# Kernel optimization log

Hardware: AMD Instinct MI355X
Metric: run time of the kernel (lower is better)

Reference implementation:

```python
import jax, jax.numpy as jnp
import numpy as np

EPS = 1e-5

def layernorm(x, g, b):
    mu = jnp.mean(x, axis=-1, keepdims=True)
    var = jnp.mean((x - mu) ** 2, axis=-1, keepdims=True)
    return (x - mu) * jax.lax.rsqrt(var + EPS) * g + b

def cswin_attn(q, k, v, lepe_w, lepe_b, H, W, H_sp, W_sp, num_heads):
    # q,k,v: (B, L, C) with C = branch dim
    B, L, C = q.shape
    d = C // num_heads
    nH, nW = H // H_sp, W // W_sp
    def to_win(t):
        t = t.transpose(0, 2, 1).reshape(B, C, nH, H_sp, nW, W_sp)
        t = t.transpose(0, 2, 4, 3, 5, 1).reshape(B * nH * nW, H_sp * W_sp, num_heads, d)
        return t.transpose(0, 2, 1, 3)  # (Bw, h, N, d)
    kw = to_win(k)
    vw = to_win(v)
    # q windows as images for LePE depthwise conv
    qi = q.transpose(0, 2, 1).reshape(B, C, nH, H_sp, nW, W_sp)
    qi = qi.transpose(0, 2, 4, 1, 3, 5).reshape(B * nH * nW, C, H_sp, W_sp)
    lepe = jax.lax.conv_general_dilated(qi, lepe_w, (1, 1), 'SAME',
                                        feature_group_count=C,
                                        dimension_numbers=('NCHW', 'OIHW', 'NCHW'))
    lepe = lepe + lepe_b[None, :, None, None]
    lepe = lepe.reshape(-1, num_heads, d, H_sp * W_sp).transpose(0, 1, 3, 2)
    qw = qi.reshape(-1, num_heads, d, H_sp * W_sp).transpose(0, 1, 3, 2) * (float(d) ** -0.5)
    attn = jax.nn.softmax(jnp.einsum('whnd,whmd->whnm', qw, kw), axis=-1)
    out = jnp.einsum('whnm,whmd->whnd', attn, vw) + lepe  # (Bw, h, N, d)
    out = out.transpose(0, 2, 1, 3).reshape(B, nH, nW, H_sp, W_sp, C)
    out = out.transpose(0, 1, 3, 2, 4, 5).reshape(B, H * W, C)
    return out

def setup_inputs() -> dict:
    key = jax.random.key(0)
    ks = jax.random.split(key, 20)
    B, C, H, W = 8, 128, 64, 64
    ch_z = 512
    hid = 4 * C
    Cb = C // 2  # branch dim
    s = lambda fin: (1.0 / np.sqrt(fin))
    inp = {
        'x': jax.random.normal(ks[0], (B, C, H, W), jnp.float32),
        'z': jax.random.normal(ks[1], (B, ch_z), jnp.float32),
        'ln1_g': jnp.ones((C,), jnp.float32), 'ln1_b': jnp.zeros((C,), jnp.float32),
        'ln2_g': jnp.ones((C,), jnp.float32), 'ln2_b': jnp.zeros((C,), jnp.float32),
        'Wz1': jax.random.normal(ks[2], (C, ch_z), jnp.float32) * s(ch_z),
        'Wz2': jax.random.normal(ks[3], (C, ch_z), jnp.float32) * s(ch_z),
        'Wqkv': jax.random.normal(ks[4], (3 * C, C), jnp.float32) * s(C),
        'Wproj': jax.random.normal(ks[5], (C, C), jnp.float32) * s(C),
        'bproj': jnp.zeros((C,), jnp.float32),
        'lepe_w0': jax.random.normal(ks[6], (Cb, 1, 3, 3), jnp.float32) * (1.0 / 3.0),
        'lepe_b0': jnp.zeros((Cb,), jnp.float32),
        'lepe_w1': jax.random.normal(ks[7], (Cb, 1, 3, 3), jnp.float32) * (1.0 / 3.0),
        'lepe_b1': jnp.zeros((Cb,), jnp.float32),
        'W1': jax.random.normal(ks[8], (hid, C), jnp.float32) * s(C),
        'b1': jnp.zeros((hid,), jnp.float32),
        'W2': jax.random.normal(ks[9], (C, hid), jnp.float32) * s(hid),
        'b2': jnp.zeros((C,), jnp.float32),
    }
    return inp

def reference(x, z, ln1_g, ln1_b, ln2_g, ln2_b, Wz1, Wz2, Wqkv, Wproj, bproj,
              lepe_w0, lepe_b0, lepe_w1, lepe_b1, W1, b1, W2, b2):
    B, C, H, W = x.shape
    nh = 4  # num_heads // 2 per branch
    ss = 8  # split_size
    Cb = C // 2
    xf = x.reshape(B, C, H * W).transpose(0, 2, 1)  # (B, L, C)
    # code-conditioned attention branch
    z1 = z @ Wz1.T  # (B, C)
    h1 = layernorm(xf, ln1_g, ln1_b) + z1[:, None, :]
    qkv = (h1 @ Wqkv.T).reshape(B, H * W, 3, C).transpose(2, 0, 1, 3)  # (3, B, L, C)
    q, k, v = qkv[0], qkv[1], qkv[2]
    x1 = cswin_attn(q[..., :Cb], k[..., :Cb], v[..., :Cb], lepe_w0, lepe_b0, H, W, H, ss, nh)
    x2 = cswin_attn(q[..., Cb:], k[..., Cb:], v[..., Cb:], lepe_w1, lepe_b1, H, W, ss, W, nh)
    att = jnp.concatenate([x1, x2], axis=2) @ Wproj.T + bproj
    xf = xf + att
    # code-conditioned MLP branch
    z2 = z @ Wz2.T
    h2 = layernorm(xf, ln2_g, ln2_b) + z2[:, None, :]
    mlp = jax.nn.gelu(h2 @ W1.T + b1, approximate=False) @ W2.T + b2
    xf = xf + mlp
    return xf.transpose(0, 2, 1).reshape(B, C, H, W)
```

## Files before the change

### kernel.cpp

```cpp
#include <hip/hip_runtime.h>
#include <cstddef>

__device__ __forceinline__ float b2f(unsigned short u) {
  return __uint_as_float(((unsigned int)u) << 16);
}
__device__ __forceinline__ unsigned short f2b(float f) {
  unsigned int u = __float_as_uint(f);
  u = u + 0x7FFFu + ((u >> 16) & 1u);
  return (unsigned short)(u >> 16);
}
__device__ __forceinline__ unsigned int cvtpk(float lo, float hi) {
  unsigned int r;
  asm("v_cvt_pk_bf16_f32 %0, %1, %2" : "=v"(r) : "v"(lo), "v"(hi));
  return r;
}
__device__ __forceinline__ float gelu_exact(float x) {
  return 0.5f * x * (1.0f + erff(x * 0.70710678118654752f));
}

#if defined(__has_builtin)
#if __has_builtin(__builtin_amdgcn_exp2f)
#define EXP2(x) __builtin_amdgcn_exp2f(x)
#else
#define EXP2(x) __expf((x) * 0.6931471805599453f)
#endif
#else
#define EXP2(x) __expf((x) * 0.6931471805599453f)
#endif

typedef __attribute__((ext_vector_type(8))) short bf16x8;
typedef __attribute__((ext_vector_type(4))) short bf16x4;
typedef __attribute__((ext_vector_type(4))) float f32x4;

#if defined(__has_builtin)
#if __has_builtin(__builtin_amdgcn_mfma_f32_16x16x16bf16_1k)
#define MFMA16(a, b, c) __builtin_amdgcn_mfma_f32_16x16x16bf16_1k(a, b, c, 0, 0, 0)
#define HAVE_MFMA16 1
#elif __has_builtin(__builtin_amdgcn_mfma_f32_16x16x16_bf16)
#define MFMA16(a, b, c) __builtin_amdgcn_mfma_f32_16x16x16_bf16(a, b, c, 0, 0, 0)
#define HAVE_MFMA16 1
#endif
#endif

__device__ __forceinline__ unsigned int dtype_flag(const unsigned short* gref) {
  return (gref[0] == 0x3F80u) ? 1u : 0u;
}

struct Ptrs18 { const void* p[18]; };
__constant__ const int c_off[19] = {
    0, 4096, 4224, 4352, 4480, 4608, 70144, 135680, 184832, 201216,
    201344, 201920, 201984, 202560, 202624, 268160, 268672, 334208, 334336};

__global__ __launch_bounds__(256) void k_front(Ptrs18 ptrs,
                                               unsigned short* __restrict__ dst,
                                               const void* __restrict__ x,
                                               const unsigned short* __restrict__ gref,
                                               float* __restrict__ xf) {
  __shared__ float t[32][33];
  int bx = blockIdx.x;
  if (bx < 1306) {
    int idx = bx * 256 + threadIdx.x;
    if (idx >= 334336) return;
    unsigned int flag = dtype_flag((const unsigned short*)ptrs.p[1]);
    int i = 0;
#pragma unroll
    for (int tt = 1; tt < 18; ++tt) i += (idx >= c_off[tt]);
    int local = idx - c_off[i];
    if (flag) dst[idx] = ((const unsigned short*)ptrs.p[i])[local];
    else      dst[idx] = f2b(((const float*)ptrs.p[i])[local]);
    return;
  }
  int lb = bx - 1306;
  unsigned int flag = dtype_flag(gref);
  int b = lb >> 9;
  int c0 = ((lb >> 7) & 3) * 32, l0 = (lb & 127) * 32;
  int tx = threadIdx.x & 31, ty = threadIdx.x >> 5;
#pragma unroll
  for (int i = 0; i < 32; i += 8) {
    size_t gi = ((size_t)b * 128 + c0 + ty + i) * 4096 + l0 + tx;
    t[ty + i][tx] = flag ? b2f(((const unsigned short*)x)[gi]) : ((const float*)x)[gi];
  }
  __syncthreads();
#pragma unroll
  for (int i = 0; i < 32; i += 8)
    xf[((size_t)b * 4096 + l0 + ty + i) * 128 + c0 + tx] = t[tx][ty + i];
}

__global__ __launch_bounds__(256) void k_zmm(const unsigned short* __restrict__ z,
                                             const unsigned short* __restrict__ Wz1,
                                             const unsigned short* __restrict__ Wz2,
                                             float* __restrict__ zz) {
  __shared__ float sz[512];
  int b = blockIdx.x, tid = threadIdx.x;
  sz[tid]       = b2f(z[b * 512 + tid]);
  sz[tid + 256] = b2f(z[b * 512 + 256 + tid]);
  __syncthreads();
  const unsigned short* W = (tid < 128) ? Wz1 : Wz2;
  int c = tid & 127;
  const unsigned short* wr = W + c * 512;
  float acc = 0.f;
  for (int k = 0; k < 512; k += 4) {
    ushort4 wv = *(const ushort4*)&wr[k];
    acc += b2f(wv.x) * sz[k] + b2f(wv.y) * sz[k + 1] + b2f(wv.z) * sz[k + 2] + b2f(wv.w) * sz[k + 3];
  }
  zz[b * 256 + tid] = acc;
}

__global__ __launch_bounds__(256) void k_ln(const float* __restrict__ x,
                                            const unsigned short* __restrict__ g,
                                            const unsigned short* __restrict__ bb,
                                            const float* __restrict__ zz, int zsel,
                                            unsigned short* __restrict__ out) {
  int row = blockIdx.x * 4 + (threadIdx.x >> 6);
  int lane = threadIdx.x & 63;
  int b = row >> 12;
  const float* xr = x + (size_t)row * 128;
  float2 v = *(const float2*)&xr[lane * 2];
  float s = v.x + v.y, s2 = v.x * v.x + v.y * v.y;
#pragma unroll
  for (int m = 32; m; m >>= 1) {
    s += __shfl_xor(s, m, 64);
    s2 += __shfl_xor(s2, m, 64);
  }
  float mu = s * 0.0078125f;
  float var = s2 * 0.0078125f - mu * mu;
  float rstd = rsqrtf(var + 1e-5f);
  int c = lane * 2;
  const float* zr = zz + b * 256 + zsel * 128;
  float ox = (v.x - mu) * rstd * b2f(g[c])     + b2f(bb[c])     + zr[c];
  float oy = (v.y - mu) * rstd * b2f(g[c + 1]) + b2f(bb[c + 1]) + zr[c + 1];
  ushort2 o2; o2.x = f2b(ox); o2.y = f2b(oy);
  *(ushort2*)&out[(size_t)row * 128 + c] = o2;
}

__global__ __launch_bounds__(256) void k_gemm_mfma(const unsigned short* __restrict__ A,
                                                   const unsigned short* __restrict__ W,
                                                   const unsigned short* __restrict__ bias,
                                                   const float* __restrict__ res,
                                                   void* __restrict__ out,
                                                   int M, int N, int K, int ldw, int flags) {
  __shared__ unsigned short As[128][136];
  int bm = blockIdx.x * 128, bn = blockIdx.y * 128;
  int tid = threadIdx.x;
  int lane = tid & 63, wv = tid >> 6;
  int wm = (wv >> 1) * 64, wn = (wv & 1) * 64;
  int qd = lane >> 4, l15 = lane & 15;
#pragma unroll
  for (int i = tid; i < 2048; i += 256) {
    int row = i >> 4, c8 = (i & 15) << 3;
    *(bf16x8*)&As[row][c8] = *(const bf16x8*)&A[(size_t)(bm + row) * 128 + c8];
  }
  __syncthreads();
  f32x4 acc[4][4] = {};
#pragma unroll
  for (int ks = 0; ks < 4; ++ks) {
    bf16x8 af[4], bfr[4];
#pragma unroll
    for (int t = 0; t < 4; ++t) {
      af[t]  = *(const bf16x8*)&As[wm + t * 16 + l15][ks * 32 + qd * 8];
      bfr[t] = *(const bf16x8*)&W[(size_t)(bn + wn + t * 16 + l15) * ldw + ks * 32 + qd * 8];
    }
#pragma unroll
    for (int mi = 0; mi < 4; ++mi)
#pragma unroll
      for (int nj = 0; nj < 4; ++nj)
        acc[mi][nj] = __builtin_amdgcn_mfma_f32_16x16x32_bf16(af[mi], bfr[nj],
                                                              acc[mi][nj], 0, 0, 0);
  }
  if (flags & 4) {
#pragma unroll
    for (int mi = 0; mi < 4; ++mi)
#pragma unroll
      for (int r = 0; r < 4; ++r) {
        int row = bm + wm + mi * 16 + qd * 4 + r;
        int bb2 = row >> 12, l = row & 4095;
        int hI = l >> 6, wI = l & 63;
        int s0 = wI >> 3, t0 = hI * 8 + (wI & 7);
        int s1 = hI >> 3, t1 = (hI & 7) * 64 + wI;
#pragma unroll
        for (int nj = 0; nj < 4; ++nj) {
          int colb = bn + wn + nj * 16;
          int kv = colb >> 7, br = (colb >> 6) & 1, hh2 = (colb >> 4) & 3;
          int ss = br ? s1 : s0, tt = br ? t1 : t0;
          size_t addr = ((((size_t)((kv * 8 + bb2) * 2 + br) * 4 + hh2) * 8 + ss) * 512 + tt) * 16 + l15;
          ((unsigned short*)out)[addr] = f2b(acc[mi][nj][r]);
        }
      }
    return;
  }
  float bv[4];
#pragma unroll
  for (int nj = 0; nj < 4; ++nj)
    bv[nj] = bias ? b2f(bias[bn + wn + nj * 16 + l15]) : 0.f;
#pragma unroll
  for (int mi = 0; mi < 4; ++mi) {
#pragma unroll
    for (int r = 0; r < 4; ++r) {
      int row = bm + wm + mi * 16 + qd * 4 + r;
#pragma unroll
      for (int nj = 0; nj < 4; ++nj) {
        int col = bn + wn + nj * 16 + l15;
        float t = acc[mi][nj][r] + bv[nj];
        if (res) t += res[(size_t)row * N + col];
        if (flags & 2) ((unsigned short*)out)[(size_t)row * N + col] = f2b(t);
        else           ((float*)out)[(size_t)row * N + col] = t;
      }
    }
  }
}

__global__ __launch_bounds__(256, 4) void k_pm(const unsigned short* __restrict__ att,
                                               const unsigned short* __restrict__ Wp,
                                               const unsigned short* __restrict__ bp,
                                               const float* __restrict__ xf,
                                               const unsigned short* __restrict__ g,
                                               const unsigned short* __restrict__ bb,
                                               const float* __restrict__ zz,
                                               const unsigned short* __restrict__ W1,
                                               const unsigned short* __restrict__ b1,
                                               const unsigned short* __restrict__ W2,
                                               const unsigned short* __restrict__ b2,
                                               const unsigned short* __restrict__ gref,
                                               void* __restrict__ outp) {
  __shared__ __align__(16) char smem[35840];
  float (*xt)[132] = (float(*)[132])smem;
  unsigned short (*As_all)[136] = (unsigned short(*)[136])(smem + 16896);
  unsigned short (*Hs)[32][40]  = (unsigned short(*)[32][40])(smem + 25600);
  int tid = threadIdx.x;
  int bm = blockIdx.x * 32;
  int bidx = bm >> 12;
  int lane = tid & 63, wv = tid >> 6;
  int qd = lane >> 4, l15 = lane & 15;
  {
    int i = tid;
    int row = i >> 4, c8 = (i & 15) << 3;
    *(bf16x8*)&As_all[row][c8] = *(const bf16x8*)&att[(size_t)(bm + row) * 128 + c8];
    i += 256; row = i >> 4; c8 = (i & 15) << 3;
    *(bf16x8*)&As_all[row][c8] = *(const bf16x8*)&att[(size_t)(bm + row) * 128 + c8];
  }
  __syncthreads();
  {
    f32x4 acc[2][2] = {};
#pragma unroll
    for (int ks = 0; ks < 4; ++ks) {
      bf16x8 af[2], bfr[2];
#pragma unroll
      for (int t = 0; t < 2; ++t)
        af[t] = *(const bf16x8*)&As_all[t * 16 + l15][ks * 32 + qd * 8];
#pragma unroll
      for (int t = 0; t < 2; ++t)
        bfr[t] = *(const bf16x8*)&Wp[(wv * 32 + t * 16 + l15) * 128 + ks * 32 + qd * 8];
#pragma unroll
      for (int mi = 0; mi < 2; ++mi)
#pragma unroll
        for (int nj = 0; nj < 2; ++nj)
          acc[mi][nj] = __builtin_amdgcn_mfma_f32_16x16x32_bf16(af[mi], bfr[nj],
                                                                acc[mi][nj], 0, 0, 0);
    }
    float bv[2];
#pragma unroll
    for (int nj = 0; nj < 2; ++nj)
      bv[nj] = b2f(bp[wv * 32 + nj * 16 + l15]);
#pragma unroll
    for (int mi = 0; mi < 2; ++mi)
#pragma unroll
      for (int r = 0; r < 4; ++r) {
        int row = mi * 16 + qd * 4 + r;
#pragma unroll
        for (int nj = 0; nj < 2; ++nj) {
          int col = wv * 32 + nj * 16 + l15;
          xt[row][col] = acc[mi][nj][r] + bv[nj] + xf[(size_t)(bm + row) * 128 + col];
        }
      }
  }
  __syncthreads();
  {
    int row = tid >> 3, part = tid & 7;
    float v[16];
#pragma unroll
    for (int i = 0; i < 4; ++i) *(float4*)&v[i * 4] = *(const float4*)&xt[row][part * 16 + i * 4];
    float s = 0.f, s2 = 0.f;
#pragma unroll
    for (int i = 0; i < 16; ++i) { s += v[i]; s2 += v[i] * v[i]; }
    s  += __shfl_xor(s, 1, 64);  s  += __shfl_xor(s, 2, 64);  s  += __shfl_xor(s, 4, 64);
    s2 += __shfl_xor(s2, 1, 64); s2 += __shfl_xor(s2, 2, 64); s2 += __shfl_xor(s2, 4, 64);
    float mu = s * 0.0078125f;
    float var = s2 * 0.0078125f - mu * mu;
    float rstd = rsqrtf(var + 1e-5f);
    const float* zr = zz + bidx * 256 + 128 + part * 16;
#pragma unroll
    for (int i = 0; i < 16; i += 2) {
      int c = part * 16 + i;
      float ox = (v[i]     - mu) * rstd * b2f(g[c])     + b2f(bb[c])     + zr[i];
      float oy = (v[i + 1] - mu) * rstd * b2f(g[c + 1]) + b2f(bb[c + 1]) + zr[i + 1];
      unsigned int u = (unsigned int)f2b(ox) | ((unsigned int)f2b(oy) << 16);
      *(unsigned int*)&As_all[row][c] = u;
    }
  }
  __syncthreads();
  f32x4 acc2[2][2] = {};
#pragma unroll 1
  for (int j = 0; j < 4; ++j) {
    f32x4 acc1[2][2] = {};
    const unsigned short* W1j = W1 + j * 128 * 128;
#pragma unroll
    for (int ks = 0; ks < 4; ++ks) {
      bf16x8 af[2], bfr[2];
#pragma unroll
      for (int t = 0; t < 2; ++t)
        af[t] = *(const bf16x8*)&As_all[t * 16 + l15][ks * 32 + qd * 8];
#pragma unroll
      for (int t = 0; t < 2; ++t)
        bfr[t] = *(const bf16x8*)&W1j[(wv * 32 + t * 16 + l15) * 128 + ks * 32 + qd * 8];
#pragma unroll
      for (int mi = 0; mi < 2; ++mi)
#pragma unroll
        for (int nj = 0; nj < 2; ++nj)
          acc1[mi][nj] = __builtin_amdgcn_mfma_f32_16x16x32_bf16(af[mi], bfr[nj],
                                                                 acc1[mi][nj], 0, 0, 0);
    }
    bf16x8 w2f[8];
#pragma unroll
    for (int ks = 0; ks < 4; ++ks)
#pragma unroll
      for (int t = 0; t < 2; ++t)
        w2f[ks * 2 + t] = *(const bf16x8*)&W2[(wv * 32 + t * 16 + l15) * 512 + j * 128 + ks * 32 + qd * 8];
    if (j) __syncthreads();
    float bv1[2];
#pragma unroll
    for (int nj = 0; nj < 2; ++nj)
      bv1[nj] = b2f(b1[j * 128 + wv * 32 + nj * 16 + l15]);
#pragma unroll
    for (int mi = 0; mi < 2; ++mi)
#pragma unroll
      for (int nj = 0; nj < 2; ++nj)
#pragma unroll
        for (int r = 0; r < 4; ++r) {
          float t = gelu_exact(acc1[mi][nj][r] + bv1[nj]);
          Hs[wv][mi * 16 + qd * 4 + r][nj * 16 + l15] = f2b(t);
        }
    __syncthreads();
#pragma unroll
    for (int ks = 0; ks < 4; ++ks) {
      bf16x8 af2[2];
#pragma unroll
      for (int t = 0; t < 2; ++t)
        af2[t] = *(const bf16x8*)&Hs[ks][t * 16 + l15][qd * 8];
#pragma unroll
      for (int mi = 0; mi < 2; ++mi)
#pragma unroll
        for (int nj = 0; nj < 2; ++nj)
          acc2[mi][nj] = __builtin_amdgcn_mfma_f32_16x16x32_bf16(af2[mi], w2f[ks * 2 + nj],
                                                                 acc2[mi][nj], 0, 0, 0);
    }
  }
  float bv2[2];
#pragma unroll
  for (int nj = 0; nj < 2; ++nj)
    bv2[nj] = b2f(b2[wv * 32 + nj * 16 + l15]);
  __syncthreads();
  float* tile = (float*)(smem + 16896);
#pragma unroll
  for (int mi = 0; mi < 2; ++mi)
#pragma unroll
    for (int r = 0; r < 4; ++r) {
      int row = mi * 16 + qd * 4 + r;
#pragma unroll
      for (int nj = 0; nj < 2; ++nj) {
        int col = wv * 32 + nj * 16 + l15;
        tile[col * 36 + row] = acc2[mi][nj][r] + bv2[nj] + xt[row][col];
      }
    }
  __syncthreads();
  unsigned int flag = dtype_flag(gref);
  int c = tid >> 1, hf = tid & 1;
  int b = bm >> 12, l0 = (bm & 4095) + hf * 16;
  const float* tr = &tile[c * 36 + hf * 16];
  if (flag) {
    unsigned short* op = (unsigned short*)outp + ((size_t)(b * 128 + c)) * 4096 + l0;
#pragma unroll
    for (int i = 0; i < 16; i += 4) {
      ushort4 o;
      o.x = f2b(tr[i]); o.y = f2b(tr[i + 1]); o.z = f2b(tr[i + 2]); o.w = f2b(tr[i + 3]);
      *(ushort4*)&op[i] = o;
    }
  } else {
    float* op = (float*)outp + ((size_t)(b * 128 + c)) * 4096 + l0;
#pragma unroll
    for (int i = 0; i < 16; i += 4)
      *(float4*)&op[i] = *(const float4*)&tr[i];
  }
}

__global__ __launch_bounds__(256, 4) void k_attn_mfma(const unsigned short* __restrict__ qkvw,
                                                      const unsigned short* __restrict__ lw0,
                                                      const unsigned short* __restrict__ lb0,
                                                      const unsigned short* __restrict__ lw1,
                                                      const unsigned short* __restrict__ lb1,
                                                      unsigned short* __restrict__ att) {
  __shared__ unsigned short Ks[512][16];
  __shared__ unsigned short Vt[16][520];
  const size_t S1 = 4194304;
  int branch = blockIdx.y;
  int bx = blockIdx.x;
  int half = bx & 1, wh = bx >> 1;
  int w = wh >> 2, hh = wh & 3;
  int b = w >> 3, s = w & 7;
  int cb = branch * 64 + hh * 16;
  size_t slab = ((size_t)(((b * 2 + branch) * 4 + hh) * 8 + s)) * 8192;
  const unsigned short* Qg = qkvw + slab;
  const unsigned short* Kg = qkvw + S1 + slab;
  const unsigned short* Vg = qkvw + 2 * S1 + slab;
  int tid = threadIdx.x;
  for (int i = tid; i < 1024; i += 256) {
    int tok = i >> 1, c8 = (i & 1) << 3;
    *(bf16x8*)&Ks[tok][c8] = *(const bf16x8*)&Kg[tok * 16 + c8];
    bf16x8 vv = *(const bf16x8*)&Vg[tok * 16 + c8];
    int col = (tok & ~31) | ((tok & 12) << 1) | ((tok & 16) >> 2) | (tok & 3);
#pragma unroll
    for (int j = 0; j < 8; ++j) Vt[c8 + j][col] = (unsigned short)vv[j];
  }
  __syncthreads();
  int lane = tid & 63, wv = tid >> 6;
  int qd = lane >> 4, l15 = lane & 15;
  int koff = (qd & 1) * 8;
  const unsigned short* lwp = branch ? lw1 : lw0;
  const unsigned short* lbp = branch ? lb1 : lb0;
  float wreg[4][9], breg[4];
#pragma unroll
  for (int r = 0; r < 4; ++r) {
    int cc = hh * 16 + qd * 4 + r;
    breg[r] = b2f(lbp[cc]);
#pragma unroll
    for (int j = 0; j < 9; ++j) wreg[r][j] = b2f(lwp[cc * 9 + j]);
  }
  bf16x8 onesv;
#pragma unroll
  for (int j = 0; j < 8; ++j) onesv[j] = (short)0x3F80;
  int sy = branch ? 64 : 8;
  int yl = branch ? 8 : 64;
  int xl = branch ? 64 : 8;
  const float QSCALE = 0.25f * 1.44269504f;
  const float NS = -11.5415603f;
  const f32x4 NSHIFT = {NS, NS, NS, NS};
#pragma unroll 1
  for (int qt = 0; qt < 4; ++qt) {
    int q0 = half * 256 + wv * 64 + qt * 16;
    int tq = q0 + l15;
#ifdef HAVE_MFMA16
    bf16x4 qf;
    {
      ushort4 raw = *(const ushort4*)&Qg[tq * 16 + qd * 4];
      qf[0] = (short)f2b(b2f(raw.x) * QSCALE);
      qf[1] = (short)f2b(b2f(raw.y) * QSCALE);
      qf[2] = (short)f2b(b2f(raw.z) * QSCALE);
      qf[3] = (short)f2b(b2f(raw.w) * QSCALE);
    }
#else
    bf16x8 qf = {};
    if (qd < 2) {
      bf16x8 raw = *(const bf16x8*)&Qg[tq * 16 + qd * 8];
#pragma unroll
      for (int j = 0; j < 8; ++j)
        qf[j] = (short)f2b(b2f((unsigned short)raw[j]) * QSCALE);
    }
#endif
    f32x4 O0 = {0.f, 0.f, 0.f, 0.f}, O1 = {0.f, 0.f, 0.f, 0.f};
    f32x4 Osum = {0.f, 0.f, 0.f, 0.f};
#pragma unroll 1
    for (int kc = 0; kc < 4; ++kc) {
      f32x4 sc[8];
#pragma unroll
      for (int c = 0; c < 8; ++c) {
#ifdef HAVE_MFMA16
        bf16x4 kf = *(const bf16x4*)&Ks[kc * 128 + c * 16 + l15][qd * 4];
        sc[c] = MFMA16(kf, qf, NSHIFT);
#else
        bf16x8 kf = *(const bf16x8*)&Ks[kc * 128 + c * 16 + l15][koff];
        sc[c] = __builtin_amdgcn_mfma_f32_16x16x32_bf16(kf, qf, NSHIFT, 0, 0, 0);
#endif
      }
#pragma unroll
      for (int c = 0; c < 8; ++c) {
        float e0 = EXP2(sc[c][0]), e1 = EXP2(sc[c][1]);
        float e2 = EXP2(sc[c][2]), e3 = EXP2(sc[c][3]);
        sc[c][0] = __uint_as_float(cvtpk(e0, e1));
        sc[c][1] = __uint_as_float(cvtpk(e2, e3));
      }
#pragma unroll
      for (int bc = 0; bc < 4; ++bc) {
        union { unsigned int u[4]; bf16x8 v; } pu;
        pu.u[0] = __float_as_uint(sc[2 * bc][0]);
        pu.u[1] = __float_as_uint(sc[2 * bc][1]);
        pu.u[2] = __float_as_uint(sc[2 * bc + 1][0]);
        pu.u[3] = __float_as_uint(sc[2 * bc + 1][1]);
        bf16x8 vf = *(const bf16x8*)&Vt[l15][kc * 128 + bc * 32 + qd * 8];
        Osum = __builtin_amdgcn_mfma_f32_16x16x32_bf16(onesv, pu.v, Osum, 0, 0, 0);
        if (bc & 1) O1 = __builtin_amdgcn_mfma_f32_16x16x32_bf16(vf, pu.v, O1, 0, 0, 0);
        else        O0 = __builtin_amdgcn_mfma_f32_16x16x32_bf16(vf, pu.v, O0, 0, 0, 0);
      }
    }
    int y = branch ? (tq >> 6) : (tq >> 3);
    int x = branch ? (tq & 63) : (tq & 7);
    float lep[4] = {breg[0], breg[1], breg[2], breg[3]};
#pragma unroll
    for (int dy = -1; dy <= 1; ++dy)
#pragma unroll
      for (int dx = -1; dx <= 1; ++dx) {
        if ((unsigned)(y + dy) < (unsigned)yl && (unsigned)(x + dx) < (unsigned)xl) {
          int tn = tq + dy * sy + dx;
          int j = (dy + 1) * 3 + (dx + 1);
          ushort4 qv = *(const ushort4*)&Qg[tn * 16 + qd * 4];
          lep[0] += wreg[0][j] * b2f(qv.x);
          lep[1] += wreg[1][j] * b2f(qv.y);
          lep[2] += wreg[2][j] * b2f(qv.z);
          lep[3] += wreg[3][j] * b2f(qv.w);
        }
      }
    float inv = 1.f / Osum[0];
    int lo = branch ? (s * 8 + y) * 64 + x : y * 64 + s * 8 + x;
    unsigned short* op = att + ((size_t)(b * 4096 + lo)) * 128 + cb + qd * 4;
    ushort4 o;
    o.x = f2b((O0[0] + O1[0]) * inv + lep[0]);
    o.y = f2b((O0[1] + O1[1]) * inv + lep[1]);
    o.z = f2b((O0[2] + O1[2]) * inv + lep[2]);
    o.w = f2b((O0[3] + O1[3]) * inv + lep[3]);
    *(ushort4*)op = o;
  }
}

extern "C" void kernel_launch(void* const* d_in, const int* in_sizes, int n_in,
                              void* d_out, int out_size, void* d_ws, size_t ws_size,
                              hipStream_t stream) {
  const size_t S = 4194304;
  float* ws = (float*)d_ws;
  float* zz = ws + 64;
  unsigned short* norm = (unsigned short*)(ws + 2112);
  float* xf = ws + 169472;
  unsigned short* h   = (unsigned short*)(ws + 169472 + S);
  unsigned short* qkv = (unsigned short*)(ws + 169472 + S + S / 2);
  unsigned short* att = h;

  const unsigned short* z     = norm + 0;
  const unsigned short* ln1g  = norm + 4096;
  const unsigned short* ln1b  = norm + 4224;
  const unsigned short* ln2g  = norm + 4352;
  const unsigned short* ln2b  = norm + 4480;
  const unsigned short* Wz1   = norm + 4608;
  const unsigned short* Wz2   = norm + 70144;
  const unsigned short* Wqkv  = norm + 135680;
  const unsigned short* Wproj = norm + 184832;
  const unsigned short* bproj = norm + 201216;
  const unsigned short* lw0   = norm + 201344;
  const unsigned short* lb0   = norm + 201920;
  const unsigned short* lw1   = norm + 201984;
  const unsigned short* lb1   = norm + 202560;
  const unsigned short* W1    = norm + 202624;
  const unsigned short* b1    = norm + 268160;
  const unsigned short* W2    = norm + 268672;
  const unsigned short* b2    = norm + 334208;

  const unsigned short* gref = (const unsigned short*)d_in[2];

  Ptrs18 ptrs;
  for (int i = 0; i < 18; ++i) ptrs.p[i] = d_in[i + 1];

  dim3 t256(256);
  k_front<<<dim3(5402), t256, 0, stream>>>(ptrs, (unsigned short*)norm,
                                           d_in[0], gref, xf);
  k_zmm<<<dim3(8), t256, 0, stream>>>(z, Wz1, Wz2, zz);
  k_ln<<<dim3(8192), t256, 0, stream>>>(xf, ln1g, ln1b, zz, 0, h);
  k_gemm_mfma<<<dim3(256, 3), t256, 0, stream>>>(h, Wqkv, nullptr, nullptr, qkv,
                                                 32768, 384, 128, 128, 2 | 4);
  k_attn_mfma<<<dim3(512, 2), t256, 0, stream>>>(qkv, lw0, lb0, lw1, lb1, att);
  k_pm<<<dim3(1024), t256, 0, stream>>>(att, Wproj, bproj, xf, ln2g, ln2b, zz,
                                        W1, b1, W2, b2, gref, d_out);
}
```

Measured before the change: 215.1 us.

## Fuse LayerNorm into transpose front kernel and shrink QKV GEMM tile

The z-projection kernel now reads raw inputs directly and runs first. The transpose front kernel then transposes full 32-row by 128-channel tiles and computes LayerNorm1 plus the z bias in the same pass, so the separate k_ln launch and its re-read of xf disappear. The QKV GEMM uses a dedicated 64-row tile kernel with a launch-bounds occupancy hint. In k_pm, W2 fragments are loaded per k-step instead of all being preloaded, which lowers register pressure at the cost of reloads inside the loop.

```diff
diff --git a/kernel.cpp b/kernel.cpp
--- a/kernel.cpp
+++ b/kernel.cpp
@@ -46,6 +46,41 @@
   return (gref[0] == 0x3F80u) ? 1u : 0u;
 }
 
+__global__ __launch_bounds__(256) void k_zmm(const void* __restrict__ z,
+                                             const void* __restrict__ Wz1,
+                                             const void* __restrict__ Wz2,
+                                             const unsigned short* __restrict__ gref,
+                                             float* __restrict__ zz) {
+  __shared__ float sz[512];
+  unsigned int flag = dtype_flag(gref);
+  int b = blockIdx.x, tid = threadIdx.x;
+  if (flag) {
+    sz[tid]       = b2f(((const unsigned short*)z)[b * 512 + tid]);
+    sz[tid + 256] = b2f(((const unsigned short*)z)[b * 512 + 256 + tid]);
+  } else {
+    sz[tid]       = ((const float*)z)[b * 512 + tid];
+    sz[tid + 256] = ((const float*)z)[b * 512 + 256 + tid];
+  }
+  __syncthreads();
+  const void* W = (tid < 128) ? Wz1 : Wz2;
+  int c = tid & 127;
+  float acc = 0.f;
+  if (flag) {
+    const unsigned short* wr = (const unsigned short*)W + c * 512;
+    for (int k = 0; k < 512; k += 4) {
+      ushort4 wv = *(const ushort4*)&wr[k];
+      acc += b2f(wv.x) * sz[k] + b2f(wv.y) * sz[k + 1] + b2f(wv.z) * sz[k + 2] + b2f(wv.w) * sz[k + 3];
+    }
+  } else {
+    const float* wr = (const float*)W + c * 512;
+    for (int k = 0; k < 512; k += 4) {
+      float4 wv = *(const float4*)&wr[k];
+      acc += wv.x * sz[k] + wv.y * sz[k + 1] + wv.z * sz[k + 2] + wv.w * sz[k + 3];
+    }
+  }
+  zz[b * 256 + tid] = acc;
+}
+
 struct Ptrs18 { const void* p[18]; };
 __constant__ const int c_off[19] = {
     0, 4096, 4224, 4352, 4480, 4608, 70144, 135680, 184832, 201216,
@@ -55,11 +90,16 @@
                                                unsigned short* __restrict__ dst,
                                                const void* __restrict__ x,
                                                const unsigned short* __restrict__ gref,
-                                               float* __restrict__ xf) {
-  __shared__ float t[32][33];
+                                               const void* __restrict__ g1,
+                                               const void* __restrict__ b1v,
+                                               const float* __restrict__ zz,
+                                               float* __restrict__ xf,
+                                               unsigned short* __restrict__ h) {
+  __shared__ float xt[32][133];
   int bx = blockIdx.x;
+  int tid = threadIdx.x;
   if (bx < 1306) {
-    int idx = bx * 256 + threadIdx.x;
+    int idx = bx * 256 + tid;
     if (idx >= 334336) return;
     unsigned int flag = dtype_flag((const unsigned short*)ptrs.p[1]);
     int i = 0;
@@ -70,143 +110,100 @@
     else      dst[idx] = f2b(((const float*)ptrs.p[i])[local]);
     return;
   }
-  int lb = bx - 1306;
+  int lt = bx - 1306;
   unsigned int flag = dtype_flag(gref);
-  int b = lb >> 9;
-  int c0 = ((lb >> 7) & 3) * 32, l0 = (lb & 127) * 32;
-  int tx = threadIdx.x & 31, ty = threadIdx.x >> 5;
-#pragma unroll
-  for (int i = 0; i < 32; i += 8) {
-    size_t gi = ((size_t)b * 128 + c0 + ty + i) * 4096 + l0 + tx;
-    t[ty + i][tx] = flag ? b2f(((const unsigned short*)x)[gi]) : ((const float*)x)[gi];
-  }
-  __syncthreads();
-#pragma unroll
-  for (int i = 0; i < 32; i += 8)
-    xf[((size_t)b * 4096 + l0 + ty + i) * 128 + c0 + tx] = t[tx][ty + i];
-}
-
-__global__ __launch_bounds__(256) void k_zmm(const unsigned short* __restrict__ z,
-                                             const unsigned short* __restrict__ Wz1,
-                                             const unsigned short* __restrict__ Wz2,
-                                             float* __restrict__ zz) {
-  __shared__ float sz[512];
-  int b = blockIdx.x, tid = threadIdx.x;
-  sz[tid]       = b2f(z[b * 512 + tid]);
-  sz[tid + 256] = b2f(z[b * 512 + 256 + tid]);
-  __syncthreads();
-  const unsigned short* W = (tid < 128) ? Wz1 : Wz2;
-  int c = tid & 127;
-  const unsigned short* wr = W + c * 512;
-  float acc = 0.f;
-  for (int k = 0; k < 512; k += 4) {
-    ushort4 wv = *(const ushort4*)&wr[k];
-    acc += b2f(wv.x) * sz[k] + b2f(wv.y) * sz[k + 1] + b2f(wv.z) * sz[k + 2] + b2f(wv.w) * sz[k + 3];
-  }
-  zz[b * 256 + tid] = acc;
-}
-
-__global__ __launch_bounds__(256) void k_ln(const float* __restrict__ x,
-                                            const unsigned short* __restrict__ g,
-                                            const unsigned short* __restrict__ bb,
-                                            const float* __restrict__ zz, int zsel,
-                                            unsigned short* __restrict__ out) {
-  int row = blockIdx.x * 4 + (threadIdx.x >> 6);
-  int lane = threadIdx.x & 63;
-  int b = row >> 12;
-  const float* xr = x + (size_t)row * 128;
-  float2 v = *(const float2*)&xr[lane * 2];
-  float s = v.x + v.y, s2 = v.x * v.x + v.y * v.y;
-#pragma unroll
-  for (int m = 32; m; m >>= 1) {
-    s += __shfl_xor(s, m, 64);
-    s2 += __shfl_xor(s2, m, 64);
-  }
+  int b = lt >> 7;
+  int l0 = (lt & 127) * 32;
+  int tx = tid & 31, ty = tid >> 5;
+#pragma unroll
+  for (int ct = 0; ct < 4; ++ct)
+#pragma unroll
+    for (int i = 0; i < 32; i += 8) {
+      size_t gi = ((size_t)b * 128 + ct * 32 + ty + i) * 4096 + l0 + tx;
+      float v = flag ? b2f(((const unsigned short*)x)[gi]) : ((const float*)x)[gi];
+      xt[tx][ct * 32 + ty + i] = v;
+    }
+  __syncthreads();
+  int row = tid >> 3, part = tid & 7;
+  float v[16];
+#pragma unroll
+  for (int i = 0; i < 4; ++i) *(float4*)&v[i * 4] = *(const float4*)&xt[row][part * 16 + i * 4];
+  float s = 0.f, s2 = 0.f;
+#pragma unroll
+  for (int i = 0; i < 16; ++i) { s += v[i]; s2 += v[i] * v[i]; }
+  s  += __shfl_xor(s, 1, 64);  s  += __shfl_xor(s, 2, 64);  s  += __shfl_xor(s, 4, 64);
+  s2 += __shfl_xor(s2, 1, 64); s2 += __shfl_xor(s2, 2, 64); s2 += __shfl_xor(s2, 4, 64);
   float mu = s * 0.0078125f;
   float var = s2 * 0.0078125f - mu * mu;
   float rstd = rsqrtf(var + 1e-5f);
-  int c = lane * 2;
-  const float* zr = zz + b * 256 + zsel * 128;
-  float ox = (v.x - mu) * rstd * b2f(g[c])     + b2f(bb[c])     + zr[c];
-  float oy = (v.y - mu) * rstd * b2f(g[c + 1]) + b2f(bb[c + 1]) + zr[c + 1];
-  ushort2 o2; o2.x = f2b(ox); o2.y = f2b(oy);
-  *(ushort2*)&out[(size_t)row * 128 + c] = o2;
-}
-
-__global__ __launch_bounds__(256) void k_gemm_mfma(const unsigned short* __restrict__ A,
-                                                   const unsigned short* __restrict__ W,
-                                                   const unsigned short* __restrict__ bias,
-                                                   const float* __restrict__ res,
-                                                   void* __restrict__ out,
-                                                   int M, int N, int K, int ldw, int flags) {
-  __shared__ unsigned short As[128][136];
-  int bm = blockIdx.x * 128, bn = blockIdx.y * 128;
+  size_t grow = (size_t)(b * 4096 + l0 + row) * 128;
+#pragma unroll
+  for (int i = 0; i < 16; i += 4)
+    *(float4*)&xf[grow + part * 16 + i] = *(const float4*)&v[i];
+  const float* zr = zz + b * 256 + part * 16;
+#pragma unroll
+  for (int i = 0; i < 16; i += 2) {
+    int c = part * 16 + i;
+    float gx = flag ? b2f(((const unsigned short*)g1)[c])     : ((const float*)g1)[c];
+    float gy = flag ? b2f(((const unsigned short*)g1)[c + 1]) : ((const float*)g1)[c + 1];
+    float bx_ = flag ? b2f(((const unsigned short*)b1v)[c])     : ((const float*)b1v)[c];
+    float by_ = flag ? b2f(((const unsigned short*)b1v)[c + 1]) : ((const float*)b1v)[c + 1];
+    float ox = (v[i]     - mu) * rstd * gx + bx_ + zr[i];
+    float oy = (v[i + 1] - mu) * rstd * gy + by_ + zr[i + 1];
+    unsigned int u = (unsigned int)f2b(ox) | ((unsigned int)f2b(oy) << 16);
+    *(unsigned int*)&h[grow + c] = u;
+  }
+}
+
+__global__ __launch_bounds__(256, 4) void k_qkv64(const unsigned short* __restrict__ A,
+                                                  const unsigned short* __restrict__ W,
+                                                  unsigned short* __restrict__ out) {
+  __shared__ unsigned short As[64][136];
+  int bm = blockIdx.x * 64, bn = blockIdx.y * 128;
   int tid = threadIdx.x;
   int lane = tid & 63, wv = tid >> 6;
-  int wm = (wv >> 1) * 64, wn = (wv & 1) * 64;
   int qd = lane >> 4, l15 = lane & 15;
 #pragma unroll
-  for (int i = tid; i < 2048; i += 256) {
+  for (int i = tid; i < 1024; i += 256) {
     int row = i >> 4, c8 = (i & 15) << 3;
     *(bf16x8*)&As[row][c8] = *(const bf16x8*)&A[(size_t)(bm + row) * 128 + c8];
   }
   __syncthreads();
-  f32x4 acc[4][4] = {};
+  f32x4 acc[4][2] = {};
 #pragma unroll
   for (int ks = 0; ks < 4; ++ks) {
-    bf16x8 af[4], bfr[4];
-#pragma unroll
-    for (int t = 0; t < 4; ++t) {
-      af[t]  = *(const bf16x8*)&As[wm + t * 16 + l15][ks * 32 + qd * 8];
-      bfr[t] = *(const bf16x8*)&W[(size_t)(bn + wn + t * 16 + l15) * ldw + ks * 32 + qd * 8];
-    }
+    bf16x8 af[4], bfr[2];
+#pragma unroll
+    for (int t = 0; t < 4; ++t)
+      af[t] = *(const bf16x8*)&As[t * 16 + l15][ks * 32 + qd * 8];
+#pragma unroll
+    for (int t = 0; t < 2; ++t)
+      bfr[t] = *(const bf16x8*)&W[(size_t)(bn + wv * 32 + t * 16 + l15) * 128 + ks * 32 + qd * 8];
 #pragma unroll
     for (int mi = 0; mi < 4; ++mi)
 #pragma unroll
-      for (int nj = 0; nj < 4; ++nj)
+      for (int nj = 0; nj < 2; ++nj)
         acc[mi][nj] = __builtin_amdgcn_mfma_f32_16x16x32_bf16(af[mi], bfr[nj],
                                                               acc[mi][nj], 0, 0, 0);
   }
-  if (flags & 4) {
-#pragma unroll
-    for (int mi = 0; mi < 4; ++mi)
-#pragma unroll
-      for (int r = 0; r < 4; ++r) {
-        int row = bm + wm + mi * 16 + qd * 4 + r;
-        int bb2 = row >> 12, l = row & 4095;
-        int hI = l >> 6, wI = l & 63;
-        int s0 = wI >> 3, t0 = hI * 8 + (wI & 7);
-        int s1 = hI >> 3, t1 = (hI & 7) * 64 + wI;
-#pragma unroll
-        for (int nj = 0; nj < 4; ++nj) {
-          int colb = bn + wn + nj * 16;
-          int kv = colb >> 7, br = (colb >> 6) & 1, hh2 = (colb >> 4) & 3;
-          int ss = br ? s1 : s0, tt = br ? t1 : t0;
-          size_t addr = ((((size_t)((kv * 8 + bb2) * 2 + br) * 4 + hh2) * 8 + ss) * 512 + tt) * 16 + l15;
-          ((unsigned short*)out)[addr] = f2b(acc[mi][nj][r]);
-        }
-      }
-    return;
-  }
-  float bv[4];
-#pragma unroll
-  for (int nj = 0; nj < 4; ++nj)
-    bv[nj] = bias ? b2f(bias[bn + wn + nj * 16 + l15]) : 0.f;
-#pragma unroll
-  for (int mi = 0; mi < 4; ++mi) {
+#pragma unroll
+  for (int mi = 0; mi < 4; ++mi)
 #pragma unroll
     for (int r = 0; r < 4; ++r) {
-      int row = bm + wm + mi * 16 + qd * 4 + r;
-#pragma unroll
-      for (int nj = 0; nj < 4; ++nj) {
-        int col = bn + wn + nj * 16 + l15;
-        float t = acc[mi][nj][r] + bv[nj];
-        if (res) t += res[(size_t)row * N + col];
-        if (flags & 2) ((unsigned short*)out)[(size_t)row * N + col] = f2b(t);
-        else           ((float*)out)[(size_t)row * N + col] = t;
-      }
-    }
-  }
+      int row = bm + mi * 16 + qd * 4 + r;
+      int bb2 = row >> 12, l = row & 4095;
+      int hI = l >> 6, wI = l & 63;
+      int s0 = wI >> 3, t0 = hI * 8 + (wI & 7);
+      int s1 = hI >> 3, t1 = (hI & 7) * 64 + wI;
+#pragma unroll
+      for (int nj = 0; nj < 2; ++nj) {
+        int colb = bn + wv * 32 + nj * 16;
+        int kv = colb >> 7, br = (colb >> 6) & 1, hh2 = (colb >> 4) & 3;
+        int ss = br ? s1 : s0, tt = br ? t1 : t0;
+        size_t addr = ((((size_t)((kv * 8 + bb2) * 2 + br) * 4 + hh2) * 8 + ss) * 512 + tt) * 16 + l15;
+        out[addr] = f2b(acc[mi][nj][r]);
+      }
+    }
 }
 
 __global__ __launch_bounds__(256, 4) void k_pm(const unsigned short* __restrict__ att,
@@ -319,12 +316,6 @@
           acc1[mi][nj] = __builtin_amdgcn_mfma_f32_16x16x32_bf16(af[mi], bfr[nj],
                                                                  acc1[mi][nj], 0, 0, 0);
     }
-    bf16x8 w2f[8];
-#pragma unroll
-    for (int ks = 0; ks < 4; ++ks)
-#pragma unroll
-      for (int t = 0; t < 2; ++t)
-        w2f[ks * 2 + t] = *(const bf16x8*)&W2[(wv * 32 + t * 16 + l15) * 512 + j * 128 + ks * 32 + qd * 8];
     if (j) __syncthreads();
     float bv1[2];
 #pragma unroll
@@ -342,15 +333,18 @@
     __syncthreads();
 #pragma unroll
     for (int ks = 0; ks < 4; ++ks) {
-      bf16x8 af2[2];
+      bf16x8 af2[2], bfr2[2];
 #pragma unroll
       for (int t = 0; t < 2; ++t)
         af2[t] = *(const bf16x8*)&Hs[ks][t * 16 + l15][qd * 8];
 #pragma unroll
+      for (int t = 0; t < 2; ++t)
+        bfr2[t] = *(const bf16x8*)&W2[(wv * 32 + t * 16 + l15) * 512 + j * 128 + ks * 32 + qd * 8];
+#pragma unroll
       for (int mi = 0; mi < 2; ++mi)
 #pragma unroll
         for (int nj = 0; nj < 2; ++nj)
-          acc2[mi][nj] = __builtin_amdgcn_mfma_f32_16x16x32_bf16(af2[mi], w2f[ks * 2 + nj],
+          acc2[mi][nj] = __builtin_amdgcn_mfma_f32_16x16x32_bf16(af2[mi], bfr2[nj],
                                                                  acc2[mi][nj], 0, 0, 0);
     }
   }
@@ -541,13 +535,8 @@
   unsigned short* qkv = (unsigned short*)(ws + 169472 + S + S / 2);
   unsigned short* att = h;
 
-  const unsigned short* z     = norm + 0;
-  const unsigned short* ln1g  = norm + 4096;
-  const unsigned short* ln1b  = norm + 4224;
   const unsigned short* ln2g  = norm + 4352;
   const unsigned short* ln2b  = norm + 4480;
-  const unsigned short* Wz1   = norm + 4608;
-  const unsigned short* Wz2   = norm + 70144;
   const unsigned short* Wqkv  = norm + 135680;
   const unsigned short* Wproj = norm + 184832;
   const unsigned short* bproj = norm + 201216;
@@ -566,12 +555,11 @@
   for (int i = 0; i < 18; ++i) ptrs.p[i] = d_in[i + 1];
 
   dim3 t256(256);
-  k_front<<<dim3(5402), t256, 0, stream>>>(ptrs, (unsigned short*)norm,
-                                           d_in[0], gref, xf);
-  k_zmm<<<dim3(8), t256, 0, stream>>>(z, Wz1, Wz2, zz);
-  k_ln<<<dim3(8192), t256, 0, stream>>>(xf, ln1g, ln1b, zz, 0, h);
-  k_gemm_mfma<<<dim3(256, 3), t256, 0, stream>>>(h, Wqkv, nullptr, nullptr, qkv,
-                                                 32768, 384, 128, 128, 2 | 4);
+  k_zmm<<<dim3(8), t256, 0, stream>>>(d_in[1], d_in[6], d_in[7], gref, zz);
+  k_front<<<dim3(2330), t256, 0, stream>>>(ptrs, (unsigned short*)norm,
+                                           d_in[0], gref, d_in[2], d_in[3], zz,
+                                           xf, h);
+  k_qkv64<<<dim3(512, 3), t256, 0, stream>>>(h, Wqkv, qkv);
   k_attn_mfma<<<dim3(512, 2), t256, 0, stream>>>(qkv, lw0, lb0, lw1, lb1, att);
   k_pm<<<dim3(1024), t256, 0, stream>>>(att, Wproj, bproj, xf, ln2g, ln2b, zz,
                                         W1, b1, W2, b2, gref, d_out);
```

New measurement: 236.0 us. 9.7% more time.
